# Kernel optimization log

Measured on AMD Instinct MI355X. Metric: run time of the kernel, lower is better.

The kernel has to match this reference:

```python
import jax, jax.numpy as jnp
import numpy as np

N_NODES = 50000


def _gcn_conv(x, src, dst, norm, W, b):
    # x: [N, F_in], src/dst: [E+N] (self loops included), norm: [E+N]
    h = x @ W                                   # [N, F_out]
    msg = h[src] * norm[:, None]                # [E+N, F_out] gather + scale
    out = jax.ops.segment_sum(msg, dst, num_segments=N_NODES)  # scatter-add
    return out + b


def _norm_coeffs(edge_index, n_nodes):
    # PyG GCNConv: add self loops, deg over dst (col), norm = d^-1/2[src]*d^-1/2[dst]
    loops = jnp.arange(n_nodes, dtype=edge_index.dtype)
    src = jnp.concatenate([edge_index[0], loops])
    dst = jnp.concatenate([edge_index[1], loops])
    deg = jax.ops.segment_sum(jnp.ones_like(dst, dtype=jnp.float32), dst,
                              num_segments=n_nodes)
    dinv = jnp.where(deg > 0, jax.lax.rsqrt(jnp.maximum(deg, 1.0)), 0.0)
    norm = dinv[src] * dinv[dst]
    return src, dst, norm


def setup_inputs() -> dict:
    key = jax.random.key(0)
    ks = jax.random.split(key, 8)
    F_in, F_hid, E = 128, 128, 600000
    x = jax.random.normal(ks[0], (N_NODES, F_in), dtype=jnp.float32)
    edge_index = jax.random.randint(ks[1], (2, E), 0, N_NODES, dtype=jnp.int32)
    s1 = 1.0 / np.sqrt(F_in)
    s2 = 1.0 / np.sqrt(F_hid)
    W1 = jax.random.uniform(ks[2], (F_in, F_hid), jnp.float32, -s1, s1)
    b1 = jnp.zeros((F_hid,), jnp.float32)
    W2 = jax.random.uniform(ks[3], (F_hid, F_hid), jnp.float32, -s2, s2)
    b2 = jnp.zeros((F_hid,), jnp.float32)
    W3 = jax.random.uniform(ks[4], (F_hid, F_hid), jnp.float32, -s2, s2)
    b3 = jnp.zeros((F_hid,), jnp.float32)
    return {"x": x, "edge_index": edge_index,
            "W1": W1, "b1": b1, "W2": W2, "b2": b2, "W3": W3, "b3": b3}


def reference(x, edge_index, W1, b1, W2, b2, W3, b3):
    src, dst, norm = _norm_coeffs(edge_index, N_NODES)
    h = jax.nn.relu(_gcn_conv(x, src, dst, norm, W1, b1))
    h = jax.nn.relu(_gcn_conv(h, src, dst, norm, W2, b2))
    h = _gcn_conv(h, src, dst, norm, W3, b3)
    # original forward returns (x, h) with x rebound to h (identical arrays)
    return (h, h)
```

## Files before the change

### kernel.cpp

```cpp
#include <hip/hip_runtime.h>

#define NNODES 50000
#define FDIM 128
#define KELL 40

typedef float f4 __attribute__((ext_vector_type(4)));
typedef float f2 __attribute__((ext_vector_type(2)));
typedef short short8 __attribute__((ext_vector_type(8)));
typedef uint uint4v __attribute__((ext_vector_type(4)));
typedef uint uint2v __attribute__((ext_vector_type(2)));

__global__ __launch_bounds__(256) void k_fill(const int* __restrict__ src,
                                              const int* __restrict__ dst,
                                              int* __restrict__ fill,
                                              int* __restrict__ col, int E) {
    int i = blockIdx.x * 256 + threadIdx.x;
    int e0 = i * 2;
    if (e0 + 1 < E) {
        int2 s2 = *(const int2*)(src + e0);
        int2 d2 = *(const int2*)(dst + e0);
        int slot0 = atomicAdd(&fill[d2.x], 1);
        int slot1 = atomicAdd(&fill[d2.y], 1);
        if (slot0 < KELL) col[d2.x * KELL + slot0] = s2.x;
        if (slot1 < KELL) col[d2.y * KELL + slot1] = s2.y;
    } else if (e0 < E) {
        int d = dst[e0];
        int slot = atomicAdd(&fill[d], 1);
        if (slot < KELL) col[d * KELL + slot] = src[e0];
    }
}

__device__ __forceinline__ void split2(float x0, float x1, unsigned& hi, unsigned& lo) {
    unsigned u0 = __float_as_uint(x0), u1 = __float_as_uint(x1);
    unsigned h0 = u0 & 0xffff0000u, h1 = u1 & 0xffff0000u;
    hi = h1 | (h0 >> 16);
    float l0 = x0 - __uint_as_float(h0);
    float l1 = x1 - __uint_as_float(h1);
    lo = (__float_as_uint(l1) & 0xffff0000u) | (__float_as_uint(l0) >> 16);
}

__device__ __forceinline__ unsigned pack2(float lo, float hi) {
    unsigned ul = __float_as_uint(lo);
    unsigned uh = __float_as_uint(hi);
    ul += 0x7fffu + ((ul >> 16) & 1u);
    uh += 0x7fffu + ((uh >> 16) & 1u);
    return (ul >> 16) | (uh & 0xffff0000u);
}

__device__ __forceinline__ f4 dec(uint2v v) {
    f4 r;
    r.x = __uint_as_float(v.x << 16);
    r.y = __uint_as_float(v.x & 0xffff0000u);
    r.z = __uint_as_float(v.y << 16);
    r.w = __uint_as_float(v.y & 0xffff0000u);
    return r;
}

__global__ __launch_bounds__(256) void k_prepw(const float* __restrict__ W1,
                                               const float* __restrict__ W2,
                                               const float* __restrict__ W3,
                                               unsigned* __restrict__ wpk) {
    int y = blockIdx.y;
    const float* W = (y == 0) ? W1 : (y == 1) ? W2 : W3;
    unsigned* dh = wpk + (size_t)y * 16384;
    unsigned* dl = dh + 8192;
    int p = blockIdx.x * 256 + threadIdx.x;
    int jp = p & 3;
    int l = (p >> 2) & 63;
    int st = p >> 8;
    int s = st >> 3, t = st & 7;
    int k0 = ((l >> 4) << 3) + (jp << 1) + (s << 5);
    int n = (t << 4) + (l & 15);
    float x0 = W[k0 * 128 + n];
    float x1 = W[(k0 + 1) * 128 + n];
    unsigned hi, lo;
    split2(x0, x1, hi, lo);
    dh[p] = hi;
    dl[p] = lo;
}

__global__ __launch_bounds__(256, 4) void k_gemm(const float* __restrict__ A,
                                                 const unsigned* __restrict__ wsrc,
                                                 unsigned* __restrict__ H, int nrows) {
    int tid = threadIdx.x;
    int w = tid >> 6, l = tid & 63;
    int m16 = l & 15, q = l >> 4;
    int rbase = blockIdx.x * 64 + w * 16;
    int row = rbase + m16;
    int rowc = row > nrows - 1 ? nrows - 1 : row;

    union u8 { unsigned u[4]; uint4v uv; short8 v; };
    u8 ah[4], al[4];
    const f4* A4 = (const f4*)A;
#pragma unroll
    for (int s = 0; s < 4; ++s) {
        f4 a0 = A4[(size_t)rowc * 32 + s * 8 + q * 2];
        f4 a1 = A4[(size_t)rowc * 32 + s * 8 + q * 2 + 1];
        split2(a0.x, a0.y, ah[s].u[0], al[s].u[0]);
        split2(a0.z, a0.w, ah[s].u[1], al[s].u[1]);
        split2(a1.x, a1.y, ah[s].u[2], al[s].u[2]);
        split2(a1.z, a1.w, ah[s].u[3], al[s].u[3]);
    }

    f4 acc[8];
#pragma unroll
    for (int t = 0; t < 8; ++t) acc[t] = (f4)0.0f;

    const uint4v* wg4 = (const uint4v*)wsrc;
#pragma unroll
    for (int s = 0; s < 4; ++s) {
#pragma unroll
        for (int t = 0; t < 8; ++t) {
            u8 bh, bl;
            bh.uv = wg4[(s * 8 + t) * 64 + l];
            bl.uv = wg4[2048 + (s * 8 + t) * 64 + l];
            acc[t] = __builtin_amdgcn_mfma_f32_16x16x32_bf16(ah[s].v, bh.v, acc[t], 0, 0, 0);
            acc[t] = __builtin_amdgcn_mfma_f32_16x16x32_bf16(al[s].v, bh.v, acc[t], 0, 0, 0);
            acc[t] = __builtin_amdgcn_mfma_f32_16x16x32_bf16(ah[s].v, bl.v, acc[t], 0, 0, 0);
        }
    }

#pragma unroll
    for (int u = 0; u < 4; ++u) {
#pragma unroll
        for (int r = 0; r < 4; ++r) {
            int rr = rbase + q * 4 + r;
            if (rr < nrows)
                H[(size_t)rr * 64 + u * 16 + m16] =
                    pack2(acc[2 * u][r], acc[2 * u + 1][r]);
        }
    }
}

__global__ __launch_bounds__(256) void k_agg(const unsigned* __restrict__ hpk,
                                             const int* __restrict__ fill,
                                             const int* __restrict__ col,
                                             const float* __restrict__ bias,
                                             float* __restrict__ out,
                                             float* __restrict__ out2, int relu) {
    int gw = (blockIdx.x * 256 + threadIdx.x) >> 6;
    int lane = threadIdx.x & 63;
    int half = lane >> 5;
    int sl = lane & 31;
    int hb = half * 32;
    int n = gw * 2 + half;
    if (n >= NNODES) return;
    int deg = fill[n];
    int c = deg < KELL ? deg : KELL;
    float di = rsqrtf(1.0f + (float)deg);

    const uint2v* h2 = (const uint2v*)hpk;
    f4 a = di * dec(h2[(size_t)n * 32 + sl]);

    int beg = n * KELL;
    {
        int cv = 0;
        float wv = 0.0f;
        if (sl < c) {
            cv = col[beg + sl];
            wv = rsqrtf(1.0f + (float)fill[cv]);
        }
        int j = 0;
#pragma unroll 1
        for (; j + 8 <= c; j += 8) {
            int s0 = __shfl(cv, hb + j);
            int s1 = __shfl(cv, hb + j + 1);
            int s2 = __shfl(cv, hb + j + 2);
            int s3 = __shfl(cv, hb + j + 3);
            int s4 = __shfl(cv, hb + j + 4);
            int s5 = __shfl(cv, hb + j + 5);
            int s6 = __shfl(cv, hb + j + 6);
            int s7 = __shfl(cv, hb + j + 7);
            float w0 = __shfl(wv, hb + j);
            float w1 = __shfl(wv, hb + j + 1);
            float w2 = __shfl(wv, hb + j + 2);
            float w3 = __shfl(wv, hb + j + 3);
            float w4 = __shfl(wv, hb + j + 4);
            float w5 = __shfl(wv, hb + j + 5);
            float w6 = __shfl(wv, hb + j + 6);
            float w7 = __shfl(wv, hb + j + 7);
            uint2v v0 = h2[(size_t)s0 * 32 + sl];
            uint2v v1 = h2[(size_t)s1 * 32 + sl];
            uint2v v2 = h2[(size_t)s2 * 32 + sl];
            uint2v v3 = h2[(size_t)s3 * 32 + sl];
            uint2v v4 = h2[(size_t)s4 * 32 + sl];
            uint2v v5 = h2[(size_t)s5 * 32 + sl];
            uint2v v6 = h2[(size_t)s6 * 32 + sl];
            uint2v v7 = h2[(size_t)s7 * 32 + sl];
            a += w0 * dec(v0); a += w1 * dec(v1); a += w2 * dec(v2); a += w3 * dec(v3);
            a += w4 * dec(v4); a += w5 * dec(v5); a += w6 * dec(v6); a += w7 * dec(v7);
        }
#pragma unroll 1
        for (; j + 4 <= c; j += 4) {
            int s0 = __shfl(cv, hb + j);
            int s1 = __shfl(cv, hb + j + 1);
            int s2 = __shfl(cv, hb + j + 2);
            int s3 = __shfl(cv, hb + j + 3);
            float w0 = __shfl(wv, hb + j);
            float w1 = __shfl(wv, hb + j + 1);
            float w2 = __shfl(wv, hb + j + 2);
            float w3 = __shfl(wv, hb + j + 3);
            uint2v v0 = h2[(size_t)s0 * 32 + sl];
            uint2v v1 = h2[(size_t)s1 * 32 + sl];
            uint2v v2 = h2[(size_t)s2 * 32 + sl];
            uint2v v3 = h2[(size_t)s3 * 32 + sl];
            a += w0 * dec(v0); a += w1 * dec(v1); a += w2 * dec(v2); a += w3 * dec(v3);
        }
#pragma unroll 1
        for (; j < c; ++j) {
            int s = __shfl(cv, hb + j);
            float wgt = __shfl(wv, hb + j);
            a += wgt * dec(h2[(size_t)s * 32 + sl]);
        }
    }

    int u = sl >> 3;
    int m = (sl & 7) * 2;
    int c0 = u * 32 + m;
    f2 b0 = *(const f2*)(bias + c0);
    f2 b1 = *(const f2*)(bias + c0 + 16);
    f2 o0, o1;
    o0.x = di * a.x + b0.x;
    o0.y = di * a.z + b0.y;
    o1.x = di * a.y + b1.x;
    o1.y = di * a.w + b1.y;
    if (relu) {
        o0.x = fmaxf(o0.x, 0.0f);
        o0.y = fmaxf(o0.y, 0.0f);
        o1.x = fmaxf(o1.x, 0.0f);
        o1.y = fmaxf(o1.y, 0.0f);
    }
    float* orow = out + (size_t)n * FDIM;
    *(f2*)(orow + c0) = o0;
    *(f2*)(orow + c0 + 16) = o1;
    if (out2) {
        float* orow2 = out2 + (size_t)n * FDIM;
        *(f2*)(orow2 + c0) = o0;
        *(f2*)(orow2 + c0 + 16) = o1;
    }
}

extern "C" void kernel_launch(void* const* d_in, const int* in_sizes, int n_in,
                              void* d_out, int out_size, void* d_ws, size_t ws_size,
                              hipStream_t stream) {
    const float* x  = (const float*)d_in[0];
    const int*   ei = (const int*)d_in[1];
    const float* W1 = (const float*)d_in[2];
    const float* b1 = (const float*)d_in[3];
    const float* W2 = (const float*)d_in[4];
    const float* b2 = (const float*)d_in[5];
    const float* W3 = (const float*)d_in[6];
    const float* b3 = (const float*)d_in[7];
    int E = in_sizes[1] / 2;
    const int* srcp = ei;
    const int* dstp = ei + E;
    float* outf = (float*)d_out;

    unsigned* hpk = (unsigned*)d_ws;
    int*      fill = (int*)(hpk + (size_t)NNODES * 64);
    int*      col  = fill + NNODES;
    unsigned* wpk  = (unsigned*)(col + (size_t)NNODES * KELL);
    float*    bufB = outf;

    (void)hipMemsetAsync(fill, 0, sizeof(int) * NNODES, stream);

    int eb = (E / 2 + 255) / 256;
    int gb = (NNODES + 63) / 64;
    int ab = (NNODES / 2 * 64 + 255) / 256;

    k_prepw<<<dim3(32, 3), 256, 0, stream>>>(W1, W2, W3, wpk);
    k_fill<<<eb, 256, 0, stream>>>(srcp, dstp, fill, col, E);

    k_gemm<<<gb, 256, 0, stream>>>(x, wpk, hpk, NNODES);
    k_agg<<<ab, 256, 0, stream>>>(hpk, fill, col, b1, bufB, nullptr, 1);
    k_gemm<<<gb, 256, 0, stream>>>(bufB, wpk + 16384, hpk, NNODES);
    k_agg<<<ab, 256, 0, stream>>>(hpk, fill, col, b2, bufB, nullptr, 1);
    k_gemm<<<gb, 256, 0, stream>>>(bufB, wpk + 32768, hpk, NNODES);
    k_agg<<<ab, 256, 0, stream>>>(hpk, fill, col, b3, outf,
                                  outf + (size_t)NNODES * FDIM, 0);
}
```

Baseline: 254.8 us.

## Fuse aggregation of layer N with GEMM of layer N+1 via shared memory

Adds a k_agg_gemm kernel in which each block aggregates 64 nodes into shared memory (bias plus ReLU), then runs the split-bf16 MFMA GEMM with the next layer's weights and writes packed bf16 features directly. This removes the fp32 intermediate write and read between aggregation and GEMM for layers 1→2 and 2→3, and cuts the launch count. In exchange each wave serially aggregates 8 node pairs, leaving fewer warps in flight to hide gather latency, and it uses about 33KB of LDS per block. The packed intermediate is ping-ponged through the output buffer.

Result: faster. 249.3 us (-2.1%).

```diff
diff --git a/kernel.cpp b/kernel.cpp
--- a/kernel.cpp
+++ b/kernel.cpp
@@ -121,39 +121,42 @@
     }
 
 #pragma unroll
-    for (int u = 0; u < 4; ++u) {
+    for (int up = 0; up < 4; ++up) {
 #pragma unroll
         for (int r = 0; r < 4; ++r) {
             int rr = rbase + q * 4 + r;
             if (rr < nrows)
-                H[(size_t)rr * 64 + u * 16 + m16] =
-                    pack2(acc[2 * u][r], acc[2 * u + 1][r]);
-        }
-    }
-}
-
-__global__ __launch_bounds__(256) void k_agg(const unsigned* __restrict__ hpk,
-                                             const int* __restrict__ fill,
-                                             const int* __restrict__ col,
-                                             const float* __restrict__ bias,
-                                             float* __restrict__ out,
-                                             float* __restrict__ out2, int relu) {
-    int gw = (blockIdx.x * 256 + threadIdx.x) >> 6;
-    int lane = threadIdx.x & 63;
-    int half = lane >> 5;
-    int sl = lane & 31;
+                H[(size_t)rr * 64 + up * 16 + m16] =
+                    pack2(acc[2 * up][r], acc[2 * up + 1][r]);
+        }
+    }
+}
+
+__global__ __launch_bounds__(256, 4) void k_agg_gemm(const unsigned* __restrict__ hin,
+                                                     const int* __restrict__ fill,
+                                                     const int* __restrict__ col,
+                                                     const float* __restrict__ bias,
+                                                     const unsigned* __restrict__ wsrc,
+                                                     unsigned* __restrict__ hout) {
+    __shared__ float As[64][132];
+    int tid = threadIdx.x;
+    int w = tid >> 6, l = tid & 63;
+    int half = l >> 5;
+    int sl = l & 31;
     int hb = half * 32;
-    int n = gw * 2 + half;
-    if (n >= NNODES) return;
-    int deg = fill[n];
-    int c = deg < KELL ? deg : KELL;
-    float di = rsqrtf(1.0f + (float)deg);
-
-    const uint2v* h2 = (const uint2v*)hpk;
-    f4 a = di * dec(h2[(size_t)n * 32 + sl]);
-
-    int beg = n * KELL;
-    {
+    int nbase = blockIdx.x * 64 + w * 16;
+
+    const uint2v* h2 = (const uint2v*)hin;
+#pragma unroll 1
+    for (int it = 0; it < 8; ++it) {
+        int n = nbase + it * 2 + half;
+        int nc = n >= NNODES ? NNODES - 1 : n;
+        int deg = fill[nc];
+        int c = deg < KELL ? deg : KELL;
+        float di = rsqrtf(1.0f + (float)deg);
+        f4 a = di * dec(h2[(size_t)nc * 32 + sl]);
+
+        int beg = nc * KELL;
         int cv = 0;
         float wv = 0.0f;
         if (sl < c) {
@@ -212,6 +215,147 @@
             float wgt = __shfl(wv, hb + j);
             a += wgt * dec(h2[(size_t)s * 32 + sl]);
         }
+
+        int u = sl >> 3;
+        int m = (sl & 7) * 2;
+        int c0 = u * 32 + m;
+        f2 b0 = *(const f2*)(bias + c0);
+        f2 b1v = *(const f2*)(bias + c0 + 16);
+        f2 o0, o1;
+        o0.x = fmaxf(di * a.x + b0.x, 0.0f);
+        o0.y = fmaxf(di * a.z + b0.y, 0.0f);
+        o1.x = fmaxf(di * a.y + b1v.x, 0.0f);
+        o1.y = fmaxf(di * a.w + b1v.y, 0.0f);
+        int rl = w * 16 + it * 2 + half;
+        *(f2*)&As[rl][c0] = o0;
+        *(f2*)&As[rl][c0 + 16] = o1;
+    }
+
+    int m16 = l & 15, q = l >> 4;
+    int rl = w * 16 + m16;
+    union u8 { unsigned u[4]; uint4v uv; short8 v; };
+    u8 ah[4], al[4];
+#pragma unroll
+    for (int s = 0; s < 4; ++s) {
+        f4 a0 = *(const f4*)&As[rl][s * 32 + q * 8];
+        f4 a1 = *(const f4*)&As[rl][s * 32 + q * 8 + 4];
+        split2(a0.x, a0.y, ah[s].u[0], al[s].u[0]);
+        split2(a0.z, a0.w, ah[s].u[1], al[s].u[1]);
+        split2(a1.x, a1.y, ah[s].u[2], al[s].u[2]);
+        split2(a1.z, a1.w, ah[s].u[3], al[s].u[3]);
+    }
+
+    f4 acc[8];
+#pragma unroll
+    for (int t = 0; t < 8; ++t) acc[t] = (f4)0.0f;
+
+    const uint4v* wg4 = (const uint4v*)wsrc;
+#pragma unroll
+    for (int s = 0; s < 4; ++s) {
+#pragma unroll
+        for (int t = 0; t < 8; ++t) {
+            u8 bh, bl;
+            bh.uv = wg4[(s * 8 + t) * 64 + l];
+            bl.uv = wg4[2048 + (s * 8 + t) * 64 + l];
+            acc[t] = __builtin_amdgcn_mfma_f32_16x16x32_bf16(ah[s].v, bh.v, acc[t], 0, 0, 0);
+            acc[t] = __builtin_amdgcn_mfma_f32_16x16x32_bf16(al[s].v, bh.v, acc[t], 0, 0, 0);
+            acc[t] = __builtin_amdgcn_mfma_f32_16x16x32_bf16(ah[s].v, bl.v, acc[t], 0, 0, 0);
+        }
+    }
+
+    int rbase = blockIdx.x * 64 + w * 16;
+#pragma unroll
+    for (int up = 0; up < 4; ++up) {
+#pragma unroll
+        for (int r = 0; r < 4; ++r) {
+            int rr = rbase + q * 4 + r;
+            if (rr < NNODES)
+                hout[(size_t)rr * 64 + up * 16 + m16] =
+                    pack2(acc[2 * up][r], acc[2 * up + 1][r]);
+        }
+    }
+}
+
+__global__ __launch_bounds__(256) void k_agg(const unsigned* __restrict__ hpk,
+                                             const int* __restrict__ fill,
+                                             const int* __restrict__ col,
+                                             const float* __restrict__ bias,
+                                             float* __restrict__ out,
+                                             float* __restrict__ out2, int relu) {
+    int gw = (blockIdx.x * 256 + threadIdx.x) >> 6;
+    int lane = threadIdx.x & 63;
+    int half = lane >> 5;
+    int sl = lane & 31;
+    int hb = half * 32;
+    int n = gw * 2 + half;
+    if (n >= NNODES) return;
+    int deg = fill[n];
+    int c = deg < KELL ? deg : KELL;
+    float di = rsqrtf(1.0f + (float)deg);
+
+    const uint2v* h2 = (const uint2v*)hpk;
+    f4 a = di * dec(h2[(size_t)n * 32 + sl]);
+
+    int beg = n * KELL;
+    {
+        int cv = 0;
+        float wv = 0.0f;
+        if (sl < c) {
+            cv = col[beg + sl];
+            wv = rsqrtf(1.0f + (float)fill[cv]);
+        }
+        int j = 0;
+#pragma unroll 1
+        for (; j + 8 <= c; j += 8) {
+            int s0 = __shfl(cv, hb + j);
+            int s1 = __shfl(cv, hb + j + 1);
+            int s2 = __shfl(cv, hb + j + 2);
+            int s3 = __shfl(cv, hb + j + 3);
+            int s4 = __shfl(cv, hb + j + 4);
+            int s5 = __shfl(cv, hb + j + 5);
+            int s6 = __shfl(cv, hb + j + 6);
+            int s7 = __shfl(cv, hb + j + 7);
+            float w0 = __shfl(wv, hb + j);
+            float w1 = __shfl(wv, hb + j + 1);
+            float w2 = __shfl(wv, hb + j + 2);
+            float w3 = __shfl(wv, hb + j + 3);
+            float w4 = __shfl(wv, hb + j + 4);
+            float w5 = __shfl(wv, hb + j + 5);
+            float w6 = __shfl(wv, hb + j + 6);
+            float w7 = __shfl(wv, hb + j + 7);
+            uint2v v0 = h2[(size_t)s0 * 32 + sl];
+            uint2v v1 = h2[(size_t)s1 * 32 + sl];
+            uint2v v2 = h2[(size_t)s2 * 32 + sl];
+            uint2v v3 = h2[(size_t)s3 * 32 + sl];
+            uint2v v4 = h2[(size_t)s4 * 32 + sl];
+            uint2v v5 = h2[(size_t)s5 * 32 + sl];
+            uint2v v6 = h2[(size_t)s6 * 32 + sl];
+            uint2v v7 = h2[(size_t)s7 * 32 + sl];
+            a += w0 * dec(v0); a += w1 * dec(v1); a += w2 * dec(v2); a += w3 * dec(v3);
+            a += w4 * dec(v4); a += w5 * dec(v5); a += w6 * dec(v6); a += w7 * dec(v7);
+        }
+#pragma unroll 1
+        for (; j + 4 <= c; j += 4) {
+            int s0 = __shfl(cv, hb + j);
+            int s1 = __shfl(cv, hb + j + 1);
+            int s2 = __shfl(cv, hb + j + 2);
+            int s3 = __shfl(cv, hb + j + 3);
+            float w0 = __shfl(wv, hb + j);
+            float w1 = __shfl(wv, hb + j + 1);
+            float w2 = __shfl(wv, hb + j + 2);
+            float w3 = __shfl(wv, hb + j + 3);
+            uint2v v0 = h2[(size_t)s0 * 32 + sl];
+            uint2v v1 = h2[(size_t)s1 * 32 + sl];
+            uint2v v2 = h2[(size_t)s2 * 32 + sl];
+            uint2v v3 = h2[(size_t)s3 * 32 + sl];
+            a += w0 * dec(v0); a += w1 * dec(v1); a += w2 * dec(v2); a += w3 * dec(v3);
+        }
+#pragma unroll 1
+        for (; j < c; ++j) {
+            int s = __shfl(cv, hb + j);
+            float wgt = __shfl(wv, hb + j);
+            a += wgt * dec(h2[(size_t)s * 32 + sl]);
+        }
     }
 
     int u = sl >> 3;
@@ -256,11 +400,11 @@
     const int* dstp = ei + E;
     float* outf = (float*)d_out;
 
-    unsigned* hpk = (unsigned*)d_ws;
-    int*      fill = (int*)(hpk + (size_t)NNODES * 64);
+    unsigned* hpkA = (unsigned*)d_ws;
+    int*      fill = (int*)(hpkA + (size_t)NNODES * 64);
     int*      col  = fill + NNODES;
     unsigned* wpk  = (unsigned*)(col + (size_t)NNODES * KELL);
-    float*    bufB = outf;
+    unsigned* hpkB = (unsigned*)outf;
 
     (void)hipMemsetAsync(fill, 0, sizeof(int) * NNODES, stream);
 
@@ -271,11 +415,9 @@
     k_prepw<<<dim3(32, 3), 256, 0, stream>>>(W1, W2, W3, wpk);
     k_fill<<<eb, 256, 0, stream>>>(srcp, dstp, fill, col, E);
 
-    k_gemm<<<gb, 256, 0, stream>>>(x, wpk, hpk, NNODES);
-    k_agg<<<ab, 256, 0, stream>>>(hpk, fill, col, b1, bufB, nullptr, 1);
-    k_gemm<<<gb, 256, 0, stream>>>(bufB, wpk + 16384, hpk, NNODES);
-    k_agg<<<ab, 256, 0, stream>>>(hpk, fill, col, b2, bufB, nullptr, 1);
-    k_gemm<<<gb, 256, 0, stream>>>(bufB, wpk + 32768, hpk, NNODES);
-    k_agg<<<ab, 256, 0, stream>>>(hpk, fill, col, b3, outf,
+    k_gemm<<<gb, 256, 0, stream>>>(x, wpk, hpkA, NNODES);
+    k_agg_gemm<<<gb, 256, 0, stream>>>(hpkA, fill, col, b1, wpk + 16384, hpkB);
+    k_agg_gemm<<<gb, 256, 0, stream>>>(hpkB, fill, col, b2, wpk + 32768, hpkA);
+    k_agg<<<ab, 256, 0, stream>>>(hpkA, fill, col, b3, outf,
                                   outf + (size_t)NNODES * FDIM, 0);
 }
```
